# Kernel optimization log

Measured on AMD Instinct MI355X. Metric: run time of the kernel, lower is better.

## Reference

```python
import jax, jax.numpy as jnp
import numpy as np

KERNEL_MUL = 2.0
KERNEL_NUM = 5


def _mmd(source, target):
    n = source.shape[0]
    total = jnp.concatenate([source, target], axis=0)          # [2N, D]
    n_samples = total.shape[0]
    # GEMM-based pairwise squared L2 distances (same math as broadcast subtract/square/sum)
    sq = jnp.sum(total * total, axis=-1)                        # [2N]
    L2 = sq[:, None] + sq[None, :] - 2.0 * (total @ total.T)    # [2N, 2N]
    # bandwidth from detached distances (torch uses .data)
    bw = jax.lax.stop_gradient(jnp.sum(L2)) / (n_samples ** 2 - n_samples)
    bw = bw / (KERNEL_MUL ** (KERNEL_NUM // 2))
    kernels = jnp.zeros_like(L2)
    for i in range(KERNEL_NUM):
        kernels = kernels + jnp.exp(-L2 / (bw * KERNEL_MUL ** i))
    XX = kernels[:n, :n]
    YY = kernels[n:, n:]
    XY = kernels[:n, n:]
    YX = kernels[n:, :n]
    return jnp.mean(XX + YY - XY - YX)


def setup_inputs() -> dict:
    key = jax.random.key(0)
    k1, k2 = jax.random.split(key)
    N, D = 4096, 128
    source = jax.random.normal(k1, (N, D), dtype=jnp.float32)
    target = jax.random.normal(k2, (N, D), dtype=jnp.float32)
    return {"source": source, "target": target}


def reference(source, target):
    return _mmd(source, target)
```

## Files before the change

kernel.cpp:

```cpp
#include <hip/hip_runtime.h>

#define D 128
#define NT2 2080
#define NPART 8320

typedef __attribute__((ext_vector_type(8))) short short8;
typedef __attribute__((ext_vector_type(4))) float float4v;
typedef __attribute__((ext_vector_type(2))) float float2v;

static __device__ __forceinline__ unsigned short f2bf(float f) {
    unsigned int u = __float_as_uint(f);
    unsigned int r = (u + 0x7fffu + ((u >> 16) & 1u)) >> 16;
    return (unsigned short)r;
}

static __device__ __forceinline__ void gld16(const void* g, void* l) {
    __builtin_amdgcn_global_load_lds(
        (const __attribute__((address_space(1))) unsigned int*)g,
        (__attribute__((address_space(3))) unsigned int*)l, 16, 0, 0);
}


__global__ __launch_bounds__(256) void k_prep(const float* __restrict__ src,
                                              const float* __restrict__ tgt,
                                              float* __restrict__ wsf,
                                              unsigned int* __restrict__ XTu) {
    if (blockIdx.x < 2048) {
        float* rowsq = wsf + 33280;
        const int wv = threadIdx.x >> 6, lane = threadIdx.x & 63;
        const int gr = blockIdx.x * 4 + wv;
        const float* Xr = (gr < 4096) ? src + (size_t)gr * D : tgt + (size_t)(gr - 4096) * D;
        float2 f = ((const float2*)Xr)[lane];
        XTu[(gr >> 4) * 1024 + (lane >> 2) * 64 + (gr & 15) * 4 + (lane & 3)] =
            (unsigned)f2bf(f.x) | ((unsigned)f2bf(f.y) << 16);
        float s = f.x * f.x + f.y * f.y;
        #pragma unroll
        for (int off = 32; off; off >>= 1) s += __shfl_down(s, off);
        if (lane == 0) rowsq[gr] = s;
    } else {
        float* colpart = wsf + 512;
        int b = blockIdx.x - 2048;
        int col = threadIdx.x & 127, half = threadIdx.x >> 7;
        const float* X = (b < 64) ? src + (size_t)(b * 64) * D
                                  : tgt + (size_t)((b - 64) * 64) * D;
        float p0 = 0.f, p1 = 0.f, p2 = 0.f, p3 = 0.f;
        #pragma unroll 4
        for (int i = 0; i < 32; i += 4) {
            p0 += X[(size_t)(2 * (i + 0) + half) * D + col];
            p1 += X[(size_t)(2 * (i + 1) + half) * D + col];
            p2 += X[(size_t)(2 * (i + 2) + half) * D + col];
            p3 += X[(size_t)(2 * (i + 3) + half) * D + col];
        }
        __shared__ float cp[2][128];
        cp[half][col] = (p0 + p1) + (p2 + p3);
        __syncthreads();
        if (threadIdx.x < 128)
            colpart[b * 128 + threadIdx.x] = cp[0][threadIdx.x] + cp[1][threadIdx.x];
    }
}

__global__ __launch_bounds__(256) void p3_consts(float* __restrict__ wsf) {
    const float* colpart = wsf + 512;
    const float* rowsq = wsf + 33280;
    const int tid = threadIdx.x, lane = tid & 63;

    float s0 = 0.f, s1 = 0.f, s2 = 0.f, s3 = 0.f;
    #pragma unroll
    for (int i = 0; i < 32; i += 4) {
        s0 += rowsq[tid + 256 * (i + 0)];
        s1 += rowsq[tid + 256 * (i + 1)];
        s2 += rowsq[tid + 256 * (i + 2)];
        s3 += rowsq[tid + 256 * (i + 3)];
    }
    float s = (s0 + s1) + (s2 + s3);
    #pragma unroll
    for (int off = 32; off; off >>= 1) s += __shfl_down(s, off);
    __shared__ float red[8];
    __shared__ float csum[128];
    if (lane == 0) red[tid >> 6] = s;

    int c = tid & 127, h = tid >> 7;
    float q0 = 0.f, q1 = 0.f, q2 = 0.f, q3 = 0.f;
    #pragma unroll 4
    for (int b = 0; b < 64; b += 4) {
        q0 += colpart[(h * 64 + b + 0) * 128 + c];
        q1 += colpart[(h * 64 + b + 1) * 128 + c];
        q2 += colpart[(h * 64 + b + 2) * 128 + c];
        q3 += colpart[(h * 64 + b + 3) * 128 + c];
    }
    float cs = (q0 + q1) + (q2 + q3);
    __syncthreads();
    if (h == 0) csum[c] = cs;
    __syncthreads();
    if (h == 1) csum[c] += cs;
    __syncthreads();
    float v = (tid < 128) ? csum[tid] * csum[tid] : 0.f;
    #pragma unroll
    for (int off = 32; off; off >>= 1) v += __shfl_down(v, off);
    if (lane == 0) red[4 + (tid >> 6)] = v;
    __syncthreads();
    if (tid == 0) {
        double ss = (double)red[0] + red[1] + red[2] + red[3];
        double s2 = (double)red[4] + red[5] + red[6] + red[7];
        double sumL2 = 2.0 * 8192.0 * ss - 2.0 * s2;
        double bw = sumL2 / (8192.0 * 8192.0 - 8192.0) / 4.0;
        wsf[4] = (float)(-1.4426950408889634 / (bw * 16.0));
    }
}

__global__ __launch_bounds__(256) void mmd_main(const uint4* __restrict__ XT,
                                                const float* __restrict__ wsf,
                                                float* __restrict__ partial) {
    __shared__ uint4 lds[4096];
    const float* rowsq = wsf + 33280;
    const int tid = threadIdx.x;
    const int lane = tid & 63, wv = tid >> 6;
    const int quad = lane >> 4, mrow = lane & 15;
    const int wm = wv >> 1, wn = wv & 1;

    int b = blockIdx.x;
    int t2 = (b & 7) * (NT2 / 8) + (b >> 3);

    int pi = (int)((129.0 - sqrt(129.0 * 129.0 - 8.0 * (double)t2)) * 0.5);
    auto base = [](int p) { return (p * (129 - p)) >> 1; };
    while (base(pi + 1) <= t2) ++pi;
    while (base(pi) > t2) --pi;
    int pj = pi + (t2 - base(pi));

    const char* gA = (const char*)(XT + (size_t)pi * 2048);
    char* lb = (char*)lds;
    #pragma unroll
    for (int it = 0; it < 8; ++it)
        gld16(gA + it * 4096 + tid * 16, lb + it * 4096 + tid * 16);
    if (pj != pi) {
        const char* gB = (const char*)(XT + (size_t)pj * 2048);
        #pragma unroll
        for (int it = 0; it < 8; ++it)
            gld16(gB + it * 4096 + tid * 16, lb + 32768 + it * 4096 + tid * 16);
    }
    const uint4* As = lds + wm * 1024;
    const uint4* Bs = ((pj != pi) ? lds + 2048 : lds) + wn * 1024;
    const int ti = pi * 2 + wm, tj = pj * 2 + wn;
    float c4 = wsf[4];

    const float* rsqA = rowsq + ti * 64;
    const float* rsqB = rowsq + tj * 64;
    float rAc[4][4], rBc[4];
    #pragma unroll
    for (int mt = 0; mt < 4; ++mt)
        #pragma unroll
        for (int r = 0; r < 4; ++r)
            rAc[mt][r] = rsqA[mt * 16 + quad * 4 + r] * c4;
    #pragma unroll
    for (int nt = 0; nt < 4; ++nt)
        rBc[nt] = rsqB[nt * 16 + mrow] * c4;

    __syncthreads();

    float4v acc[4][4];
    #pragma unroll
    for (int mt = 0; mt < 4; ++mt)
        #pragma unroll
        for (int nt = 0; nt < 4; ++nt)
            acc[mt][nt] = (float4v){0.f, 0.f, 0.f, 0.f};

    #pragma unroll
    for (int kc = 0; kc < 4; ++kc) {
        short8 af[4], bf[4];
        #pragma unroll
        for (int mt = 0; mt < 4; ++mt)
            af[mt] = *(const short8*)&As[mt * 256 + kc * 64 + lane];
        #pragma unroll
        for (int nt = 0; nt < 4; ++nt)
            bf[nt] = *(const short8*)&Bs[nt * 256 + kc * 64 + lane];
        #pragma unroll
        for (int mt = 0; mt < 4; ++mt)
            #pragma unroll
            for (int nt = 0; nt < 4; ++nt)
                acc[mt][nt] = __builtin_amdgcn_mfma_f32_16x16x32_bf16(af[mt], bf[nt], acc[mt][nt], 0, 0, 0);
    }

    const float cm2 = -2.f * c4;
    const float2v cm2v = {cm2, cm2};
    float2v part2 = {0.f, 0.f};
    #pragma unroll
    for (int mt = 0; mt < 4; ++mt) {
        const float2v rA01 = { rAc[mt][0], rAc[mt][1] };
        const float2v rA23 = { rAc[mt][2], rAc[mt][3] };
        #pragma unroll
        for (int nt = 0; nt < 4; ++nt) {
            const float2v rB2 = {rBc[nt], rBc[nt]};
            float4v d = acc[mt][nt];
            float2v d01 = {d[0], d[1]}, d23 = {d[2], d[3]};
            float2v a01 = d01 * cm2v + (rA01 + rB2);
            float2v a23 = d23 * cm2v + (rA23 + rB2);
            float2v e1a = { __builtin_amdgcn_exp2f(a01[0]), __builtin_amdgcn_exp2f(a01[1]) };
            float2v e1b = { __builtin_amdgcn_exp2f(a23[0]), __builtin_amdgcn_exp2f(a23[1]) };
            float2v e2a = e1a * e1a, e4a = e2a * e2a, e8a = e4a * e4a, e16a = e8a * e8a;
            float2v e2b = e1b * e1b, e4b = e2b * e2b, e8b = e4b * e4b, e16b = e8b * e8b;
            part2 += (e1a + e2a) + ((e4a + e8a) + e16a);
            part2 += (e1b + e2b) + ((e4b + e8b) + e16b);
        }
    }
    float part = part2[0] + part2[1];
    #pragma unroll
    for (int off = 32; off; off >>= 1) part += __shfl_down(part, off);

    if (lane == 0) {
        float wgt;
        if (pi == pj) {
            if (wm == 1 && wn == 0) wgt = 0.f;
            else wgt = (ti == tj) ? 1.f : 2.f;
        } else {
            wgt = ((pi < 32) == (pj < 32)) ? 2.f : -2.f;
        }
        partial[t2 * 4 + wv] = wgt * part;
    }
}

__global__ __launch_bounds__(256) void f_final(const float* __restrict__ wsf,
                                               float* __restrict__ out) {
    const float* partial = wsf + 41472;
    int tid = threadIdx.x, lane = tid & 63;
    double a0 = 0.0, a1 = 0.0, a2 = 0.0, a3 = 0.0;
    #pragma unroll 4
    for (int i = tid; i < NPART; i += 1024) {
        a0 += (double)partial[i];
        if (i + 256 < NPART) a1 += (double)partial[i + 256];
        if (i + 512 < NPART) a2 += (double)partial[i + 512];
        if (i + 768 < NPART) a3 += (double)partial[i + 768];
    }
    double s = (a0 + a1) + (a2 + a3);
    #pragma unroll
    for (int off = 32; off; off >>= 1) s += __shfl_down(s, off);
    __shared__ double r4[4];
    if (lane == 0) r4[tid >> 6] = s;
    __syncthreads();
    if (tid == 0)
        out[0] = (float)(((r4[0] + r4[1]) + (r4[2] + r4[3])) * (1.0 / (4096.0 * 4096.0)));
}

extern "C" void kernel_launch(void* const* d_in, const int* in_sizes, int n_in,
                              void* d_out, int out_size, void* d_ws, size_t ws_size,
                              hipStream_t stream) {
    const float* src = (const float*)d_in[0];
    const float* tgt = (const float*)d_in[1];
    float* wsf = (float*)d_ws;
    unsigned int* XTu = (unsigned int*)(wsf + 65536);
    float* partial = wsf + 41472;

    hipLaunchKernelGGL(k_prep, dim3(2176), dim3(256), 0, stream, src, tgt, wsf, XTu);
    hipLaunchKernelGGL(p3_consts, dim3(1), dim3(256), 0, stream, wsf);
    hipLaunchKernelGGL(mmd_main, dim3(NT2), dim3(256), 0, stream,
                       (const uint4*)XTu, wsf, partial);
    hipLaunchKernelGGL(f_final, dim3(1), dim3(256), 0, stream, wsf, (float*)d_out);
}
```

Baseline: 92.92 us.

## Use 8-wave blocks with B fragments loaded directly from global into registers

The main kernel now runs 512 threads per block split into 8 waves, each computing a 64x32 sub-tile instead of 64x64. Only the A panel is staged in LDS, which halves LDS use per block; each wave loads its B fragments straight from global memory into registers. The aim is higher occupancy, less LDS traffic and more latency hiding. The cost is redundant global B loads across the two row-waves, fewer MFMAs per wave to amortize overhead, and twice as many partial sums for the final reduction.

```diff
diff --git a/kernel.cpp b/kernel.cpp
--- a/kernel.cpp
+++ b/kernel.cpp
@@ -2,7 +2,7 @@
 
 #define D 128
 #define NT2 2080
-#define NPART 8320
+#define NPART 16640
 
 typedef __attribute__((ext_vector_type(8))) short short8;
 typedef __attribute__((ext_vector_type(4))) float float4v;
@@ -108,15 +108,15 @@
     }
 }
 
-__global__ __launch_bounds__(256) void mmd_main(const uint4* __restrict__ XT,
-                                                const float* __restrict__ wsf,
-                                                float* __restrict__ partial) {
-    __shared__ uint4 lds[4096];
+__global__ __launch_bounds__(512, 4) void mmd_main(const uint4* __restrict__ XT,
+                                                   const float* __restrict__ wsf,
+                                                   float* __restrict__ partial) {
+    __shared__ uint4 Alds[2048];
     const float* rowsq = wsf + 33280;
     const int tid = threadIdx.x;
     const int lane = tid & 63, wv = tid >> 6;
     const int quad = lane >> 4, mrow = lane & 15;
-    const int wm = wv >> 1, wn = wv & 1;
+    const int wm = wv >> 2, wn = wv & 3;
 
     int b = blockIdx.x;
     int t2 = (b & 7) * (NT2 / 8) + (b >> 3);
@@ -128,56 +128,51 @@
     int pj = pi + (t2 - base(pi));
 
     const char* gA = (const char*)(XT + (size_t)pi * 2048);
-    char* lb = (char*)lds;
-    #pragma unroll
-    for (int it = 0; it < 8; ++it)
-        gld16(gA + it * 4096 + tid * 16, lb + it * 4096 + tid * 16);
-    if (pj != pi) {
-        const char* gB = (const char*)(XT + (size_t)pj * 2048);
-        #pragma unroll
-        for (int it = 0; it < 8; ++it)
-            gld16(gB + it * 4096 + tid * 16, lb + 32768 + it * 4096 + tid * 16);
-    }
-    const uint4* As = lds + wm * 1024;
-    const uint4* Bs = ((pj != pi) ? lds + 2048 : lds) + wn * 1024;
-    const int ti = pi * 2 + wm, tj = pj * 2 + wn;
+    char* lA = (char*)Alds;
+    #pragma unroll
+    for (int it = 0; it < 4; ++it)
+        gld16(gA + it * 8192 + tid * 16, lA + it * 8192 + tid * 16);
+
+    const uint4* Bg = XT + (size_t)pj * 2048 + (wn * 2) * 256;
+    short8 bfh[4][2];
+    #pragma unroll
+    for (int kc = 0; kc < 4; ++kc) {
+        bfh[kc][0] = *(const short8*)&Bg[kc * 64 + lane];
+        bfh[kc][1] = *(const short8*)&Bg[256 + kc * 64 + lane];
+    }
+
     float c4 = wsf[4];
-
-    const float* rsqA = rowsq + ti * 64;
-    const float* rsqB = rowsq + tj * 64;
-    float rAc[4][4], rBc[4];
+    float rAc[4][4], rBc[2];
     #pragma unroll
     for (int mt = 0; mt < 4; ++mt)
         #pragma unroll
         for (int r = 0; r < 4; ++r)
-            rAc[mt][r] = rsqA[mt * 16 + quad * 4 + r] * c4;
-    #pragma unroll
-    for (int nt = 0; nt < 4; ++nt)
-        rBc[nt] = rsqB[nt * 16 + mrow] * c4;
-
-    __syncthreads();
-
-    float4v acc[4][4];
+            rAc[mt][r] = rowsq[pi * 128 + wm * 64 + mt * 16 + quad * 4 + r] * c4;
+    #pragma unroll
+    for (int nt = 0; nt < 2; ++nt)
+        rBc[nt] = rowsq[pj * 128 + wn * 32 + nt * 16 + mrow] * c4;
+
+    __syncthreads();
+
+    const uint4* As = Alds + wm * 1024;
+    float4v acc[4][2];
     #pragma unroll
     for (int mt = 0; mt < 4; ++mt)
         #pragma unroll
-        for (int nt = 0; nt < 4; ++nt)
+        for (int nt = 0; nt < 2; ++nt)
             acc[mt][nt] = (float4v){0.f, 0.f, 0.f, 0.f};
 
     #pragma unroll
     for (int kc = 0; kc < 4; ++kc) {
-        short8 af[4], bf[4];
+        short8 af[4];
         #pragma unroll
         for (int mt = 0; mt < 4; ++mt)
             af[mt] = *(const short8*)&As[mt * 256 + kc * 64 + lane];
         #pragma unroll
-        for (int nt = 0; nt < 4; ++nt)
-            bf[nt] = *(const short8*)&Bs[nt * 256 + kc * 64 + lane];
-        #pragma unroll
         for (int mt = 0; mt < 4; ++mt)
             #pragma unroll
-            for (int nt = 0; nt < 4; ++nt)
-                acc[mt][nt] = __builtin_amdgcn_mfma_f32_16x16x32_bf16(af[mt], bf[nt], acc[mt][nt], 0, 0, 0);
+            for (int nt = 0; nt < 2; ++nt)
+                acc[mt][nt] = __builtin_amdgcn_mfma_f32_16x16x32_bf16(af[mt], bfh[kc][nt], acc[mt][nt], 0, 0, 0);
     }
 
     const float cm2 = -2.f * c4;
@@ -188,7 +183,7 @@
         const float2v rA01 = { rAc[mt][0], rAc[mt][1] };
         const float2v rA23 = { rAc[mt][2], rAc[mt][3] };
         #pragma unroll
-        for (int nt = 0; nt < 4; ++nt) {
+        for (int nt = 0; nt < 2; ++nt) {
             const float2v rB2 = {rBc[nt], rBc[nt]};
             float4v d = acc[mt][nt];
             float2v d01 = {d[0], d[1]}, d23 = {d[2], d[3]};
@@ -209,12 +204,13 @@
     if (lane == 0) {
         float wgt;
         if (pi == pj) {
-            if (wm == 1 && wn == 0) wgt = 0.f;
-            else wgt = (ti == tj) ? 1.f : 2.f;
+            if (wm == 1 && wn < 2) wgt = 0.f;
+            else if ((wm == 0 && wn < 2) || (wm == 1 && wn >= 2)) wgt = 1.f;
+            else wgt = 2.f;
         } else {
             wgt = ((pi < 32) == (pj < 32)) ? 2.f : -2.f;
         }
-        partial[t2 * 4 + wv] = wgt * part;
+        partial[t2 * 8 + wv] = wgt * part;
     }
 }
 
@@ -251,7 +247,7 @@
 
     hipLaunchKernelGGL(k_prep, dim3(2176), dim3(256), 0, stream, src, tgt, wsf, XTu);
     hipLaunchKernelGGL(p3_consts, dim3(1), dim3(256), 0, stream, wsf);
-    hipLaunchKernelGGL(mmd_main, dim3(NT2), dim3(256), 0, stream,
+    hipLaunchKernelGGL(mmd_main, dim3(NT2), dim3(512), 0, stream,
                        (const uint4*)XTu, wsf, partial);
     hipLaunchKernelGGL(f_final, dim3(1), dim3(256), 0, stream, wsf, (float*)d_out);
 }
```

Measured after the change: 100.4 us. +8.0%, slower.

## Process two column tiles per block, reusing A tile and prefetching second B

Applied to the files above, without the earlier changes.

Each block now handles two adjacent upper-triangle tile pairs (pi,pj0) and (pi,pj0+1), so the A tile is loaded into LDS once and reused. The grid shrinks from 2080 to 1056 blocks. The second B tile is loaded asynchronously into LDS while the first tile's exp epilogue runs. Fewer blocks may lower occupancy and load balance across CUs, and the pair index now comes from a serial loop.

```diff
diff --git a/kernel.cpp b/kernel.cpp
--- a/kernel.cpp
+++ b/kernel.cpp
@@ -1,7 +1,7 @@
 #include <hip/hip_runtime.h>
 
 #define D 128
-#define NT2 2080
+#define NPAIR 1056
 #define NPART 8320
 
 typedef __attribute__((ext_vector_type(8))) short short8;
@@ -111,110 +111,132 @@
 __global__ __launch_bounds__(256) void mmd_main(const uint4* __restrict__ XT,
                                                 const float* __restrict__ wsf,
                                                 float* __restrict__ partial) {
-    __shared__ uint4 lds[4096];
+    __shared__ uint4 Alds[2048];
+    __shared__ uint4 Blds[2048];
     const float* rowsq = wsf + 33280;
     const int tid = threadIdx.x;
     const int lane = tid & 63, wv = tid >> 6;
     const int quad = lane >> 4, mrow = lane & 15;
     const int wm = wv >> 1, wn = wv & 1;
 
-    int b = blockIdx.x;
-    int t2 = (b & 7) * (NT2 / 8) + (b >> 3);
-
-    int pi = (int)((129.0 - sqrt(129.0 * 129.0 - 8.0 * (double)t2)) * 0.5);
-    auto base = [](int p) { return (p * (129 - p)) >> 1; };
-    while (base(pi + 1) <= t2) ++pi;
-    while (base(pi) > t2) --pi;
-    int pj = pi + (t2 - base(pi));
+    const int pairid = (blockIdx.x & 7) * (NPAIR / 8) + (blockIdx.x >> 3);
+
+    int rem = pairid, pi = 0;
+    while (rem >= ((65 - pi) >> 1)) { rem -= (65 - pi) >> 1; ++pi; }
+    const int pj0 = pi + 2 * rem;
+    const bool has2 = (pj0 < 63);
+    const int pj1 = pj0 + 1;
+    const bool diag = (pj0 == pi);
 
     const char* gA = (const char*)(XT + (size_t)pi * 2048);
-    char* lb = (char*)lds;
+    char* lA = (char*)Alds;
     #pragma unroll
     for (int it = 0; it < 8; ++it)
-        gld16(gA + it * 4096 + tid * 16, lb + it * 4096 + tid * 16);
-    if (pj != pi) {
-        const char* gB = (const char*)(XT + (size_t)pj * 2048);
+        gld16(gA + it * 4096 + tid * 16, lA + it * 4096 + tid * 16);
+    const int firstB = diag ? (has2 ? pj1 : -1) : pj0;
+    if (firstB >= 0) {
+        const char* gB = (const char*)(XT + (size_t)firstB * 2048);
+        char* lB = (char*)Blds;
         #pragma unroll
         for (int it = 0; it < 8; ++it)
-            gld16(gB + it * 4096 + tid * 16, lb + 32768 + it * 4096 + tid * 16);
-    }
-    const uint4* As = lds + wm * 1024;
-    const uint4* Bs = ((pj != pi) ? lds + 2048 : lds) + wn * 1024;
-    const int ti = pi * 2 + wm, tj = pj * 2 + wn;
-    float c4 = wsf[4];
-
-    const float* rsqA = rowsq + ti * 64;
-    const float* rsqB = rowsq + tj * 64;
-    float rAc[4][4], rBc[4];
-    #pragma unroll
-    for (int mt = 0; mt < 4; ++mt)
-        #pragma unroll
-        for (int r = 0; r < 4; ++r)
-            rAc[mt][r] = rsqA[mt * 16 + quad * 4 + r] * c4;
-    #pragma unroll
-    for (int nt = 0; nt < 4; ++nt)
-        rBc[nt] = rsqB[nt * 16 + mrow] * c4;
-
-    __syncthreads();
-
-    float4v acc[4][4];
-    #pragma unroll
-    for (int mt = 0; mt < 4; ++mt)
-        #pragma unroll
-        for (int nt = 0; nt < 4; ++nt)
-            acc[mt][nt] = (float4v){0.f, 0.f, 0.f, 0.f};
-
-    #pragma unroll
-    for (int kc = 0; kc < 4; ++kc) {
-        short8 af[4], bf[4];
-        #pragma unroll
-        for (int mt = 0; mt < 4; ++mt)
-            af[mt] = *(const short8*)&As[mt * 256 + kc * 64 + lane];
-        #pragma unroll
-        for (int nt = 0; nt < 4; ++nt)
-            bf[nt] = *(const short8*)&Bs[nt * 256 + kc * 64 + lane];
-        #pragma unroll
-        for (int mt = 0; mt < 4; ++mt)
-            #pragma unroll
-            for (int nt = 0; nt < 4; ++nt)
-                acc[mt][nt] = __builtin_amdgcn_mfma_f32_16x16x32_bf16(af[mt], bf[nt], acc[mt][nt], 0, 0, 0);
-    }
-
+            gld16(gB + it * 4096 + tid * 16, lB + it * 4096 + tid * 16);
+    }
+
+    const float c4 = wsf[4];
     const float cm2 = -2.f * c4;
     const float2v cm2v = {cm2, cm2};
-    float2v part2 = {0.f, 0.f};
-    #pragma unroll
-    for (int mt = 0; mt < 4; ++mt) {
-        const float2v rA01 = { rAc[mt][0], rAc[mt][1] };
-        const float2v rA23 = { rAc[mt][2], rAc[mt][3] };
-        #pragma unroll
-        for (int nt = 0; nt < 4; ++nt) {
-            const float2v rB2 = {rBc[nt], rBc[nt]};
-            float4v d = acc[mt][nt];
-            float2v d01 = {d[0], d[1]}, d23 = {d[2], d[3]};
-            float2v a01 = d01 * cm2v + (rA01 + rB2);
-            float2v a23 = d23 * cm2v + (rA23 + rB2);
-            float2v e1a = { __builtin_amdgcn_exp2f(a01[0]), __builtin_amdgcn_exp2f(a01[1]) };
-            float2v e1b = { __builtin_amdgcn_exp2f(a23[0]), __builtin_amdgcn_exp2f(a23[1]) };
-            float2v e2a = e1a * e1a, e4a = e2a * e2a, e8a = e4a * e4a, e16a = e8a * e8a;
-            float2v e2b = e1b * e1b, e4b = e2b * e2b, e8b = e4b * e4b, e16b = e8b * e8b;
-            part2 += (e1a + e2a) + ((e4a + e8a) + e16a);
-            part2 += (e1b + e2b) + ((e4b + e8b) + e16b);
-        }
-    }
-    float part = part2[0] + part2[1];
-    #pragma unroll
-    for (int off = 32; off; off >>= 1) part += __shfl_down(part, off);
-
-    if (lane == 0) {
-        float wgt;
-        if (pi == pj) {
-            if (wm == 1 && wn == 0) wgt = 0.f;
-            else wgt = (ti == tj) ? 1.f : 2.f;
-        } else {
-            wgt = ((pi < 32) == (pj < 32)) ? 2.f : -2.f;
-        }
-        partial[t2 * 4 + wv] = wgt * part;
+    float rAc[4][4], rB0c[4], rB1c[4];
+    #pragma unroll
+    for (int mt = 0; mt < 4; ++mt)
+        #pragma unroll
+        for (int rr = 0; rr < 4; ++rr)
+            rAc[mt][rr] = rowsq[pi * 128 + wm * 64 + mt * 16 + quad * 4 + rr] * c4;
+    #pragma unroll
+    for (int nt = 0; nt < 4; ++nt) {
+        rB0c[nt] = rowsq[pj0 * 128 + wn * 64 + nt * 16 + mrow] * c4;
+        rB1c[nt] = has2 ? rowsq[pj1 * 128 + wn * 64 + nt * 16 + mrow] * c4 : 0.f;
+    }
+
+    const uint4* As = Alds + wm * 1024;
+    float4v acc[4][4];
+
+    auto kc_loop = [&](const uint4* Bs) {
+        #pragma unroll
+        for (int mt = 0; mt < 4; ++mt)
+            #pragma unroll
+            for (int nt = 0; nt < 4; ++nt)
+                acc[mt][nt] = (float4v){0.f, 0.f, 0.f, 0.f};
+        #pragma unroll
+        for (int kc = 0; kc < 4; ++kc) {
+            short8 af[4], bf[4];
+            #pragma unroll
+            for (int mt = 0; mt < 4; ++mt)
+                af[mt] = *(const short8*)&As[mt * 256 + kc * 64 + lane];
+            #pragma unroll
+            for (int nt = 0; nt < 4; ++nt)
+                bf[nt] = *(const short8*)&Bs[nt * 256 + kc * 64 + lane];
+            #pragma unroll
+            for (int mt = 0; mt < 4; ++mt)
+                #pragma unroll
+                for (int nt = 0; nt < 4; ++nt)
+                    acc[mt][nt] = __builtin_amdgcn_mfma_f32_16x16x32_bf16(af[mt], bf[nt], acc[mt][nt], 0, 0, 0);
+        }
+    };
+
+    auto epi_store = [&](const float rBcL[4], int pj) {
+        float2v part2 = {0.f, 0.f};
+        #pragma unroll
+        for (int mt = 0; mt < 4; ++mt) {
+            const float2v rA01 = { rAc[mt][0], rAc[mt][1] };
+            const float2v rA23 = { rAc[mt][2], rAc[mt][3] };
+            #pragma unroll
+            for (int nt = 0; nt < 4; ++nt) {
+                const float2v rB2 = {rBcL[nt], rBcL[nt]};
+                float4v d = acc[mt][nt];
+                float2v d01 = {d[0], d[1]}, d23 = {d[2], d[3]};
+                float2v a01 = d01 * cm2v + (rA01 + rB2);
+                float2v a23 = d23 * cm2v + (rA23 + rB2);
+                float2v e1a = { __builtin_amdgcn_exp2f(a01[0]), __builtin_amdgcn_exp2f(a01[1]) };
+                float2v e1b = { __builtin_amdgcn_exp2f(a23[0]), __builtin_amdgcn_exp2f(a23[1]) };
+                float2v e2a = e1a * e1a, e4a = e2a * e2a, e8a = e4a * e4a, e16a = e8a * e8a;
+                float2v e2b = e1b * e1b, e4b = e2b * e2b, e8b = e4b * e4b, e16b = e8b * e8b;
+                part2 += (e1a + e2a) + ((e4a + e8a) + e16a);
+                part2 += (e1b + e2b) + ((e4b + e8b) + e16b);
+            }
+        }
+        float part = part2[0] + part2[1];
+        #pragma unroll
+        for (int off = 32; off; off >>= 1) part += __shfl_down(part, off);
+        if (lane == 0) {
+            float wgt;
+            if (pi == pj) {
+                if (wm == 1 && wn == 0) wgt = 0.f;
+                else wgt = (wm == wn) ? 1.f : 2.f;
+            } else {
+                wgt = ((pi < 32) == (pj < 32)) ? 2.f : -2.f;
+            }
+            const int t2 = ((pi * (129 - pi)) >> 1) + (pj - pi);
+            partial[t2 * 4 + wv] = wgt * part;
+        }
+    };
+
+    __syncthreads();
+
+    kc_loop((diag ? Alds : Blds) + wn * 1024);
+    if (has2 && !diag) {
+        __syncthreads();
+        const char* gB = (const char*)(XT + (size_t)pj1 * 2048);
+        char* lB = (char*)Blds;
+        #pragma unroll
+        for (int it = 0; it < 8; ++it)
+            gld16(gB + it * 4096 + tid * 16, lB + it * 4096 + tid * 16);
+    }
+    epi_store(rB0c, pj0);
+
+    if (has2) {
+        __syncthreads();
+        kc_loop(Blds + wn * 1024);
+        epi_store(rB1c, pj1);
     }
 }
 
@@ -251,7 +273,7 @@
 
     hipLaunchKernelGGL(k_prep, dim3(2176), dim3(256), 0, stream, src, tgt, wsf, XTu);
     hipLaunchKernelGGL(p3_consts, dim3(1), dim3(256), 0, stream, wsf);
-    hipLaunchKernelGGL(mmd_main, dim3(NT2), dim3(256), 0, stream,
+    hipLaunchKernelGGL(mmd_main, dim3(NPAIR), dim3(256), 0, stream,
                        (const uint4*)XTu, wsf, partial);
     hipLaunchKernelGGL(f_final, dim3(1), dim3(256), 0, stream, wsf, (float*)d_out);
 }
```

After: 95.41 us. 1.03x slower.
